# Performance work log

Hardware: AMD Instinct MI355X
Metric: run time of the kernel (lower is better)

Reference implementation:

```python
import jax, jax.numpy as jnp
import numpy as np

N = 50000          # num nodes
E = 800000         # num edges (avg degree 16)
F_IN = 512         # num_feature
HID = 128          # hid
COM_LAMBDA = 1.0


def setup_inputs() -> dict:
    key = jax.random.key(0)
    k1, k2, k3, k4, k5, k6 = jax.random.split(key, 6)
    v_ori_vals = jax.random.uniform(k1, (E,), dtype=jnp.float32)
    feat = jax.random.normal(k2, (N, F_IN), dtype=jnp.float32)
    v_indices = jax.random.randint(k3, (2, E), 0, N, dtype=jnp.int64)
    # GraphConvolution params
    gcn_w = jax.random.normal(k4, (F_IN, HID), dtype=jnp.float32) / np.sqrt(F_IN)
    gcn_b = jnp.zeros((HID,), dtype=jnp.float32)
    # gen_mlp: Linear(2*hid, 1), xavier_normal init
    std = 1.414 * np.sqrt(2.0 / (2 * HID + 1))
    mlp_w = jax.random.normal(k5, (1, 2 * HID), dtype=jnp.float32) * std
    mlp_b = jnp.zeros((1,), dtype=jnp.float32)
    return {"v_ori_vals": v_ori_vals, "feat": feat, "v_indices": v_indices,
            "num_node": N, "gcn_w": gcn_w, "gcn_b": gcn_b,
            "mlp_w": mlp_w, "mlp_b": mlp_b}


def reference(v_ori_vals, feat, v_indices, num_node, gcn_w, gcn_b, mlp_w, mlp_b):
    row, col = v_indices[0], v_indices[1]
    # gen_gcn: emb = A @ (feat @ W) + b  (SpMM via segment_sum over edges)
    support = feat @ gcn_w                                      # [N, HID]
    emb = jax.ops.segment_sum(v_ori_vals[:, None] * support[col], row,
                              num_segments=num_node) + gcn_b    # [N, HID]
    # gather endpoints, concat, edge-scoring MLP (dropout = identity in eval)
    ff = jnp.concatenate([emb[row], emb[col]], axis=-1)         # [E, 2*HID]
    temp = (ff @ mlp_w.T + mlp_b).reshape(-1)                   # [E]
    # sparse row-wise softmax over columns (dim=1) -> segment softmax by row
    m = jax.ops.segment_max(temp, row, num_segments=num_node)   # [N]
    e = jnp.exp(temp - m[row])                                  # [E]
    s = jax.ops.segment_sum(e, row, num_segments=num_node)      # [N]
    pi = e / s[row]                                             # [E]
    # gen_v = v_ori + com_lambda * pi (values on the shared edge pattern)
    return v_ori_vals + COM_LAMBDA * pi
```

## Files before the change

kernel.cpp:

```cpp
#include <hip/hip_runtime.h>


typedef unsigned int u32;

#define RPB     128
#define CAP     3072
#define NB_MAX  512
#define SB      256

__global__ void k_prep(const float* __restrict__ W, const float* __restrict__ mw,
                       float* __restrict__ u2, u32* __restrict__ cnt,
                       int F, int H, int nb) {
  if (blockIdx.x == 0)
    for (int s = threadIdx.x; s < nb; s += blockDim.x) cnt[s] = 0;
  int f = blockIdx.x * blockDim.x + threadIdx.x;
  if (f >= F) return;
  const float* wr = W + (size_t)f * H;
  float s = 0.f;
  for (int h = 0; h < H; ++h) s = fmaf(wr[h], mw[H + h], s);
  u2[f] = s;
}

template <int F>
__global__ void k_gemv(const float* __restrict__ feat, const float* __restrict__ u2,
                       float* __restrict__ q, int N) {
  const int lane = threadIdx.x & 63;
  const int sub  = lane & 15;
  const int grp  = lane >> 4;
  const int wid  = (blockIdx.x * blockDim.x + threadIdx.x) >> 6;
  const int r    = wid * 4 + grp;
  float4 uf[F / 64];
#pragma unroll
  for (int i = 0; i < F / 64; ++i)
    uf[i] = *(const float4*)(u2 + i * 64 + sub * 4);
  float a = 0.f;
  if (r < N) {
    const float* fr = feat + (size_t)r * F;
#pragma unroll
    for (int i = 0; i < F / 64; ++i) {
      float4 v = *(const float4*)(fr + i * 64 + sub * 4);
      a = fmaf(v.x, uf[i].x, fmaf(v.y, uf[i].y,
          fmaf(v.z, uf[i].z, fmaf(v.w, uf[i].w, a))));
    }
  }
  a += __shfl_xor(a, 8);
  a += __shfl_xor(a, 4);
  a += __shfl_xor(a, 2);
  a += __shfl_xor(a, 1);
  if (sub == 0 && r < N) q[r] = a;
}

__global__ void __launch_bounds__(1024)
k_sortscatter(const int* __restrict__ row, const int* __restrict__ col,
              const float* __restrict__ v, int E, int chunk,
              u32* __restrict__ cnt, uint2* __restrict__ rec8,
              u32* __restrict__ recE, int nb) {
  __shared__ u32 h[NB_MAX];
  __shared__ u32 start[NB_MAX];
  const int tid = threadIdx.x;
  for (int s = tid; s < nb; s += blockDim.x) h[s] = 0;
  __syncthreads();
  const int lo = blockIdx.x * chunk;
  const int hi = min(E, lo + chunk);
  for (int e = lo + tid; e < hi; e += blockDim.x)
    atomicAdd(&h[row[e] >> 7], 1u);
  __syncthreads();
  for (int s = tid; s < nb; s += blockDim.x) {
    u32 c = h[s];
    start[s] = c ? atomicAdd(&cnt[s], c) : 0u;
    h[s] = 0u;
  }
  __syncthreads();
  for (int e = lo + tid; e < hi; e += blockDim.x) {
    int r = row[e];
    int b = r >> 7;
    u32 rank = atomicAdd(&h[b], 1u);
    u32 slot = (u32)b * CAP + start[b] + rank;
    rec8[slot] = make_uint2(((u32)col[e] << 7) | (u32)(r & 127),
                            __float_as_uint(v[e]));
    recE[slot] = (u32)e;
  }
}

__global__ void __launch_bounds__(1024)
k_sum_t(const uint2* __restrict__ rec8, const u32* __restrict__ cnt,
        const float* __restrict__ q, float* __restrict__ t) {
  __shared__ float acc[RPB];
  const int b = blockIdx.x;
  const int tid = threadIdx.x;
  if (tid < RPB) acc[tid] = 0.f;
  __syncthreads();
  const u32 lo = (u32)b * CAP;
  const u32 hi = lo + min(cnt[b], (u32)CAP);
  for (u32 i = lo + tid; i < hi; i += blockDim.x) {
    uint2 rr = rec8[i];
    atomicAdd(&acc[rr.x & 127], q[rr.x >> 7] * __uint_as_float(rr.y));
  }
  __syncthreads();
  if (tid < RPB) t[b * RPB + tid] = __expf(acc[tid]);
}

__global__ void __launch_bounds__(1024)
k_sum_S_out(const uint2* __restrict__ rec8, const u32* __restrict__ recE,
            const u32* __restrict__ cnt, const float* __restrict__ t,
            const float* __restrict__ vori, float* __restrict__ out) {
  __shared__ float acc[RPB];
  const int b = blockIdx.x;
  const int tid = threadIdx.x;
  if (tid < RPB) acc[tid] = 0.f;
  __syncthreads();
  const u32 lo = (u32)b * CAP;
  const u32 hi = lo + min(cnt[b], (u32)CAP);
  for (u32 i = lo + tid; i < hi; i += blockDim.x) {
    uint2 rr = rec8[i];
    atomicAdd(&acc[rr.x & 127], t[rr.x >> 7]);
  }
  __syncthreads();
  if (tid < RPB) acc[tid] = 1.0f / acc[tid];
  __syncthreads();
  for (u32 i = lo + tid; i < hi; i += blockDim.x) {
    uint2 rr = rec8[i];
    u32 e = recE[i];
    out[e] = vori[e] + t[rr.x >> 7] * acc[rr.x & 127];
  }
}

__global__ void k_scatter_B_at(const int* __restrict__ row, const int* __restrict__ col,
                               const float* __restrict__ v, const float* __restrict__ q,
                               float* __restrict__ B, int E) {
  int e = blockIdx.x * blockDim.x + threadIdx.x;
  if (e >= E) return;
  atomicAdd(&B[row[e]], v[e] * q[col[e]]);
}
__global__ void k_node_t(const float* __restrict__ B, float* __restrict__ t, int N) {
  int n = blockIdx.x * blockDim.x + threadIdx.x;
  if (n < N) t[n] = __expf(B[n]);
}
__global__ void k_scatter_S_at(const int* __restrict__ row, const int* __restrict__ col,
                               const float* __restrict__ t, float* __restrict__ S, int E) {
  int e = blockIdx.x * blockDim.x + threadIdx.x;
  if (e >= E) return;
  atomicAdd(&S[row[e]], t[col[e]]);
}
__global__ void k_out_fb(const int* __restrict__ row, const int* __restrict__ col,
                         const float* __restrict__ vori, const float* __restrict__ t,
                         const float* __restrict__ S, float* __restrict__ out, int E) {
  int e = blockIdx.x * blockDim.x + threadIdx.x;
  if (e >= E) return;
  out[e] = vori[e] + t[col[e]] / S[row[e]];
}

extern "C" void kernel_launch(void* const* d_in, const int* in_sizes, int n_in,
                              void* d_out, int out_size, void* d_ws, size_t ws_size,
                              hipStream_t stream) {
  const float* vori = (const float*)d_in[0];
  const float* feat = (const float*)d_in[1];
  const int*   vind = (const int*)d_in[2];
  const float* W    = (const float*)d_in[4];
  const float* mw   = (const float*)d_in[6];

  const int E = in_sizes[0];
  const int H = in_sizes[6] / 2;
  const int F = in_sizes[4] / H;
  const int N = in_sizes[1] / F;

  const int* row = vind;
  const int* col = vind + E;

  const int nb   = (N + RPB - 1) / RPB;
  const int npad = nb * RPB;

  float* ws   = (float*)d_ws;
  float* u2   = ws;
  float* q    = u2 + F;
  float* t    = q + N;
  u32*   cnt  = (u32*)(t + npad);
  size_t hdr  = (size_t)((char*)(cnt + nb) - (char*)d_ws);
  hdr = (hdr + 15) & ~(size_t)15;
  uint2* rec8 = (uint2*)((char*)d_ws + hdr);
  u32*  recE  = (u32*)(rec8 + (size_t)nb * CAP);
  size_t need = hdr + (size_t)nb * CAP * 12u;

  k_prep<<<(F + 255) / 256, 256, 0, stream>>>(W, mw, u2, cnt, F, H, nb);
  k_gemv<512><<<(N + 15) / 16, 256, 0, stream>>>(feat, u2, q, N);

  if (ws_size >= need && F == 512 && nb <= NB_MAX) {
    const int chunk = (E + SB - 1) / SB;
    k_sortscatter<<<SB, 1024, 0, stream>>>(row, col, vori, E, chunk,
                                           cnt, rec8, recE, nb);
    k_sum_t<<<nb, 1024, 0, stream>>>(rec8, cnt, q, t);
    k_sum_S_out<<<nb, 1024, 0, stream>>>(rec8, recE, cnt, t, vori,
                                         (float*)d_out);
  } else {
    const int eb  = (E + 255) / 256;
    const int nbk = (N + 255) / 256;
    float* S = t + npad;
    hipMemsetAsync((void*)S, 0, sizeof(float) * (size_t)npad, stream);
    float* B = S;
    k_scatter_B_at<<<eb, 256, 0, stream>>>(row, col, vori, q, B, E);
    k_node_t<<<nbk, 256, 0, stream>>>(B, t, N);
    hipMemsetAsync((void*)S, 0, sizeof(float) * (size_t)npad, stream);
    k_scatter_S_at<<<eb, 256, 0, stream>>>(row, col, t, S, E);
    k_out_fb<<<eb, 256, 0, stream>>>(row, col, vori, t, S, (float*)d_out, E);
  }
}
```

Before: 246.9 us.

## Fuse all stages into one cooperative persistent kernel with grid syncs

Replaces the five-kernel pipeline (prep, gemv, sort-scatter, sum_t, sum_S_out) with a single cooperative kernel that runs 256 blocks of 1024 threads and separates the stages with grid.sync(). It drops the per-edge recE index buffer and writes the output with a direct per-edge pass that uses a stored inverse row sum. The aim is to remove launch gaps and the extra index traffic. In exchange it adds grid-wide barriers, runs the gemv and the per-bucket passes with a fixed, lower block count, and makes the final pass do random gathers on col and row.

```diff
diff --git a/kernel.cpp b/kernel.cpp
--- a/kernel.cpp
+++ b/kernel.cpp
@@ -1,4 +1,7 @@
 #include <hip/hip_runtime.h>
+#include <hip/hip_cooperative_groups.h>
+
+namespace cg = cooperative_groups;
 
 
 typedef unsigned int u32;
@@ -6,125 +9,153 @@
 #define RPB     128
 #define CAP     3072
 #define NB_MAX  512
-#define SB      256
-
-__global__ void k_prep(const float* __restrict__ W, const float* __restrict__ mw,
-                       float* __restrict__ u2, u32* __restrict__ cnt,
-                       int F, int H, int nb) {
-  if (blockIdx.x == 0)
-    for (int s = threadIdx.x; s < nb; s += blockDim.x) cnt[s] = 0;
+#define MBLK    256
+#define MTHR    1024
+
+template <int F>
+__global__ void __launch_bounds__(MTHR, 1)
+k_mega(const int* __restrict__ row, const int* __restrict__ col,
+       const float* __restrict__ vori, const float* __restrict__ feat,
+       const float* __restrict__ W, const float* __restrict__ mw,
+       float* __restrict__ u2, float* __restrict__ q,
+       float* __restrict__ t, float* __restrict__ invS,
+       u32* __restrict__ cnt, uint2* __restrict__ rec8,
+       float* __restrict__ out, int E, int N, int H, int nb) {
+  cg::grid_group grid = cg::this_grid();
+  const int tid  = threadIdx.x;
+  const int gtid = blockIdx.x * blockDim.x + tid;
+  const int gsz  = gridDim.x * blockDim.x;
+
+  __shared__ u32 h[NB_MAX];
+  __shared__ u32 start[NB_MAX];
+  __shared__ float acc[RPB];
+
+  for (int s = gtid; s < nb; s += gsz) cnt[s] = 0;
+  for (int f = gtid; f < F; f += gsz) {
+    const float* wr = W + (size_t)f * H;
+    float s = 0.f;
+    for (int hh = 0; hh < H; ++hh) s = fmaf(wr[hh], mw[H + hh], s);
+    u2[f] = s;
+  }
+  __threadfence();
+  grid.sync();
+
+  {
+    const int lane = tid & 63;
+    const int sub  = lane & 15;
+    const int grp  = lane >> 4;
+    const int wid  = gtid >> 6;
+    const int nwav = gsz >> 6;
+    float4 uf[F / 64];
+#pragma unroll
+    for (int i = 0; i < F / 64; ++i)
+      uf[i] = *(const float4*)(u2 + i * 64 + sub * 4);
+    for (int quad = wid; quad * 4 < N; quad += nwav) {
+      int r = quad * 4 + grp;
+      float a = 0.f;
+      if (r < N) {
+        const float* fr = feat + (size_t)r * F;
+#pragma unroll
+        for (int i = 0; i < F / 64; ++i) {
+          float4 v4 = *(const float4*)(fr + i * 64 + sub * 4);
+          a = fmaf(v4.x, uf[i].x, fmaf(v4.y, uf[i].y,
+              fmaf(v4.z, uf[i].z, fmaf(v4.w, uf[i].w, a))));
+        }
+      }
+      a += __shfl_xor(a, 8);
+      a += __shfl_xor(a, 4);
+      a += __shfl_xor(a, 2);
+      a += __shfl_xor(a, 1);
+      if (sub == 0 && r < N) q[r] = a;
+    }
+  }
+  __threadfence();
+  grid.sync();
+
+  {
+    const int chunk = (E + gridDim.x - 1) / gridDim.x;
+    for (int s = tid; s < nb; s += blockDim.x) h[s] = 0;
+    __syncthreads();
+    const int lo = blockIdx.x * chunk;
+    const int hi = min(E, lo + chunk);
+    for (int e = lo + tid; e < hi; e += blockDim.x)
+      atomicAdd(&h[row[e] >> 7], 1u);
+    __syncthreads();
+    for (int s = tid; s < nb; s += blockDim.x) {
+      u32 c = h[s];
+      start[s] = c ? atomicAdd(&cnt[s], c) : 0u;
+      h[s] = 0u;
+    }
+    __syncthreads();
+    for (int e = lo + tid; e < hi; e += blockDim.x) {
+      int r = row[e];
+      int b = r >> 7;
+      u32 rank = atomicAdd(&h[b], 1u);
+      u32 off  = min(start[b] + rank, (u32)CAP - 1);
+      rec8[(size_t)b * CAP + off] =
+          make_uint2(((u32)col[e] << 7) | (u32)(r & 127),
+                     __float_as_uint(vori[e]));
+    }
+  }
+  __threadfence();
+  grid.sync();
+
+  for (int b = blockIdx.x; b < nb; b += gridDim.x) {
+    if (tid < RPB) acc[tid] = 0.f;
+    __syncthreads();
+    const u32 lo = (u32)b * CAP;
+    const u32 n  = min(cnt[b], (u32)CAP);
+    for (u32 i = tid; i < n; i += blockDim.x) {
+      uint2 rr = rec8[lo + i];
+      atomicAdd(&acc[rr.x & 127], q[rr.x >> 7] * __uint_as_float(rr.y));
+    }
+    __syncthreads();
+    if (tid < RPB) t[b * RPB + tid] = __expf(acc[tid]);
+    __syncthreads();
+  }
+  __threadfence();
+  grid.sync();
+
+  for (int b = blockIdx.x; b < nb; b += gridDim.x) {
+    if (tid < RPB) acc[tid] = 0.f;
+    __syncthreads();
+    const u32 lo = (u32)b * CAP;
+    const u32 n  = min(cnt[b], (u32)CAP);
+    for (u32 i = tid; i < n; i += blockDim.x) {
+      uint2 rr = rec8[lo + i];
+      atomicAdd(&acc[rr.x & 127], t[rr.x >> 7]);
+    }
+    __syncthreads();
+    if (tid < RPB) invS[b * RPB + tid] = 1.0f / acc[tid];
+    __syncthreads();
+  }
+  __threadfence();
+  grid.sync();
+
+  for (int e = gtid; e < E; e += gsz)
+    out[e] = vori[e] + t[col[e]] * invS[row[e]];
+}
+
+__global__ void k_prep_fb(const float* __restrict__ W, const float* __restrict__ mw,
+                          float* __restrict__ u2, int F, int H) {
   int f = blockIdx.x * blockDim.x + threadIdx.x;
   if (f >= F) return;
   const float* wr = W + (size_t)f * H;
   float s = 0.f;
-  for (int h = 0; h < H; ++h) s = fmaf(wr[h], mw[H + h], s);
+  for (int hh = 0; hh < H; ++hh) s = fmaf(wr[hh], mw[H + hh], s);
   u2[f] = s;
 }
-
-template <int F>
-__global__ void k_gemv(const float* __restrict__ feat, const float* __restrict__ u2,
-                       float* __restrict__ q, int N) {
+__global__ void k_gemv_fb(const float* __restrict__ feat, const float* __restrict__ u2,
+                          float* __restrict__ q, int N, int F) {
   const int lane = threadIdx.x & 63;
-  const int sub  = lane & 15;
-  const int grp  = lane >> 4;
-  const int wid  = (blockIdx.x * blockDim.x + threadIdx.x) >> 6;
-  const int r    = wid * 4 + grp;
-  float4 uf[F / 64];
-#pragma unroll
-  for (int i = 0; i < F / 64; ++i)
-    uf[i] = *(const float4*)(u2 + i * 64 + sub * 4);
+  const int wave = (blockIdx.x * blockDim.x + threadIdx.x) >> 6;
+  if (wave >= N) return;
+  const float* fr = feat + (size_t)wave * F;
   float a = 0.f;
-  if (r < N) {
-    const float* fr = feat + (size_t)r * F;
-#pragma unroll
-    for (int i = 0; i < F / 64; ++i) {
-      float4 v = *(const float4*)(fr + i * 64 + sub * 4);
-      a = fmaf(v.x, uf[i].x, fmaf(v.y, uf[i].y,
-          fmaf(v.z, uf[i].z, fmaf(v.w, uf[i].w, a))));
-    }
-  }
-  a += __shfl_xor(a, 8);
-  a += __shfl_xor(a, 4);
-  a += __shfl_xor(a, 2);
-  a += __shfl_xor(a, 1);
-  if (sub == 0 && r < N) q[r] = a;
-}
-
-__global__ void __launch_bounds__(1024)
-k_sortscatter(const int* __restrict__ row, const int* __restrict__ col,
-              const float* __restrict__ v, int E, int chunk,
-              u32* __restrict__ cnt, uint2* __restrict__ rec8,
-              u32* __restrict__ recE, int nb) {
-  __shared__ u32 h[NB_MAX];
-  __shared__ u32 start[NB_MAX];
-  const int tid = threadIdx.x;
-  for (int s = tid; s < nb; s += blockDim.x) h[s] = 0;
-  __syncthreads();
-  const int lo = blockIdx.x * chunk;
-  const int hi = min(E, lo + chunk);
-  for (int e = lo + tid; e < hi; e += blockDim.x)
-    atomicAdd(&h[row[e] >> 7], 1u);
-  __syncthreads();
-  for (int s = tid; s < nb; s += blockDim.x) {
-    u32 c = h[s];
-    start[s] = c ? atomicAdd(&cnt[s], c) : 0u;
-    h[s] = 0u;
-  }
-  __syncthreads();
-  for (int e = lo + tid; e < hi; e += blockDim.x) {
-    int r = row[e];
-    int b = r >> 7;
-    u32 rank = atomicAdd(&h[b], 1u);
-    u32 slot = (u32)b * CAP + start[b] + rank;
-    rec8[slot] = make_uint2(((u32)col[e] << 7) | (u32)(r & 127),
-                            __float_as_uint(v[e]));
-    recE[slot] = (u32)e;
-  }
-}
-
-__global__ void __launch_bounds__(1024)
-k_sum_t(const uint2* __restrict__ rec8, const u32* __restrict__ cnt,
-        const float* __restrict__ q, float* __restrict__ t) {
-  __shared__ float acc[RPB];
-  const int b = blockIdx.x;
-  const int tid = threadIdx.x;
-  if (tid < RPB) acc[tid] = 0.f;
-  __syncthreads();
-  const u32 lo = (u32)b * CAP;
-  const u32 hi = lo + min(cnt[b], (u32)CAP);
-  for (u32 i = lo + tid; i < hi; i += blockDim.x) {
-    uint2 rr = rec8[i];
-    atomicAdd(&acc[rr.x & 127], q[rr.x >> 7] * __uint_as_float(rr.y));
-  }
-  __syncthreads();
-  if (tid < RPB) t[b * RPB + tid] = __expf(acc[tid]);
-}
-
-__global__ void __launch_bounds__(1024)
-k_sum_S_out(const uint2* __restrict__ rec8, const u32* __restrict__ recE,
-            const u32* __restrict__ cnt, const float* __restrict__ t,
-            const float* __restrict__ vori, float* __restrict__ out) {
-  __shared__ float acc[RPB];
-  const int b = blockIdx.x;
-  const int tid = threadIdx.x;
-  if (tid < RPB) acc[tid] = 0.f;
-  __syncthreads();
-  const u32 lo = (u32)b * CAP;
-  const u32 hi = lo + min(cnt[b], (u32)CAP);
-  for (u32 i = lo + tid; i < hi; i += blockDim.x) {
-    uint2 rr = rec8[i];
-    atomicAdd(&acc[rr.x & 127], t[rr.x >> 7]);
-  }
-  __syncthreads();
-  if (tid < RPB) acc[tid] = 1.0f / acc[tid];
-  __syncthreads();
-  for (u32 i = lo + tid; i < hi; i += blockDim.x) {
-    uint2 rr = rec8[i];
-    u32 e = recE[i];
-    out[e] = vori[e] + t[rr.x >> 7] * acc[rr.x & 127];
-  }
-}
-
+  for (int i = lane; i < F; i += 64) a = fmaf(fr[i], u2[i], a);
+  for (int off = 32; off; off >>= 1) a += __shfl_xor(a, off);
+  if (lane == 0) q[wave] = a;
+}
 __global__ void k_scatter_B_at(const int* __restrict__ row, const int* __restrict__ col,
                                const float* __restrict__ v, const float* __restrict__ q,
                                float* __restrict__ B, int E) {
@@ -153,54 +184,56 @@
 extern "C" void kernel_launch(void* const* d_in, const int* in_sizes, int n_in,
                               void* d_out, int out_size, void* d_ws, size_t ws_size,
                               hipStream_t stream) {
-  const float* vori = (const float*)d_in[0];
-  const float* feat = (const float*)d_in[1];
-  const int*   vind = (const int*)d_in[2];
-  const float* W    = (const float*)d_in[4];
-  const float* mw   = (const float*)d_in[6];
+  const int*   row_p  = (const int*)d_in[2];
+  const float* vori_p = (const float*)d_in[0];
+  const float* feat_p = (const float*)d_in[1];
+  const float* W_p    = (const float*)d_in[4];
+  const float* mw_p   = (const float*)d_in[6];
 
   const int E = in_sizes[0];
   const int H = in_sizes[6] / 2;
   const int F = in_sizes[4] / H;
   const int N = in_sizes[1] / F;
 
-  const int* row = vind;
-  const int* col = vind + E;
+  const int* col_p = row_p + E;
 
   const int nb   = (N + RPB - 1) / RPB;
   const int npad = nb * RPB;
 
   float* ws   = (float*)d_ws;
-  float* u2   = ws;
-  float* q    = u2 + F;
-  float* t    = q + N;
-  u32*   cnt  = (u32*)(t + npad);
-  size_t hdr  = (size_t)((char*)(cnt + nb) - (char*)d_ws);
+  float* u2_p = ws;
+  float* q_p  = u2_p + F;
+  float* t_p  = q_p + N;
+  float* iS_p = t_p + npad;
+  u32*  cnt_p = (u32*)(iS_p + npad);
+  size_t hdr  = (size_t)((char*)(cnt_p + nb) - (char*)d_ws);
   hdr = (hdr + 15) & ~(size_t)15;
-  uint2* rec8 = (uint2*)((char*)d_ws + hdr);
-  u32*  recE  = (u32*)(rec8 + (size_t)nb * CAP);
-  size_t need = hdr + (size_t)nb * CAP * 12u;
-
-  k_prep<<<(F + 255) / 256, 256, 0, stream>>>(W, mw, u2, cnt, F, H, nb);
-  k_gemv<512><<<(N + 15) / 16, 256, 0, stream>>>(feat, u2, q, N);
+  uint2* rec_p = (uint2*)((char*)d_ws + hdr);
+  size_t need  = hdr + (size_t)nb * CAP * sizeof(uint2);
 
   if (ws_size >= need && F == 512 && nb <= NB_MAX) {
-    const int chunk = (E + SB - 1) / SB;
-    k_sortscatter<<<SB, 1024, 0, stream>>>(row, col, vori, E, chunk,
-                                           cnt, rec8, recE, nb);
-    k_sum_t<<<nb, 1024, 0, stream>>>(rec8, cnt, q, t);
-    k_sum_S_out<<<nb, 1024, 0, stream>>>(rec8, recE, cnt, t, vori,
-                                         (float*)d_out);
+    float* out_p = (float*)d_out;
+    int E_ = E, N_ = N, H_ = H, nb_ = nb;
+    void* args[] = {
+      (void*)&row_p, (void*)&col_p, (void*)&vori_p, (void*)&feat_p,
+      (void*)&W_p,   (void*)&mw_p,  (void*)&u2_p,   (void*)&q_p,
+      (void*)&t_p,   (void*)&iS_p,  (void*)&cnt_p,  (void*)&rec_p,
+      (void*)&out_p, (void*)&E_,    (void*)&N_,     (void*)&H_,
+      (void*)&nb_
+    };
+    hipLaunchCooperativeKernel((const void*)k_mega<512>, dim3(MBLK), dim3(MTHR),
+                               args, 0, stream);
   } else {
     const int eb  = (E + 255) / 256;
     const int nbk = (N + 255) / 256;
-    float* S = t + npad;
+    float* S = iS_p;
+    k_prep_fb<<<(F + 255) / 256, 256, 0, stream>>>(W_p, mw_p, u2_p, F, H);
+    k_gemv_fb<<<(N * 64 + 255) / 256, 256, 0, stream>>>(feat_p, u2_p, q_p, N, F);
     hipMemsetAsync((void*)S, 0, sizeof(float) * (size_t)npad, stream);
-    float* B = S;
-    k_scatter_B_at<<<eb, 256, 0, stream>>>(row, col, vori, q, B, E);
-    k_node_t<<<nbk, 256, 0, stream>>>(B, t, N);
+    k_scatter_B_at<<<eb, 256, 0, stream>>>(row_p, col_p, vori_p, q_p, S, E);
+    k_node_t<<<nbk, 256, 0, stream>>>(S, t_p, N);
     hipMemsetAsync((void*)S, 0, sizeof(float) * (size_t)npad, stream);
-    k_scatter_S_at<<<eb, 256, 0, stream>>>(row, col, t, S, E);
-    k_out_fb<<<eb, 256, 0, stream>>>(row, col, vori, t, S, (float*)d_out, E);
-  }
-}
+    k_scatter_S_at<<<eb, 256, 0, stream>>>(row_p, col_p, t_p, S, E);
+    k_out_fb<<<eb, 256, 0, stream>>>(row_p, col_p, vori_p, t_p, S, (float*)d_out, E);
+  }
+}
```

Measured after the change: 831.9 us. 3.37x slower.

## Drop edge-id records, write output in edge order, use grid-stride GEMV

Applied to the files above, without the earlier changes.

Removes the per-edge recE index array from the bucketed records. The final pass now computes 1/S per node in a reduction kernel and writes the output in a separate coalesced edge-order kernel that gathers t[col] and invS[row], replacing the scattered out[e] writes. The GEMV now gives one whole wavefront per feature row with a fixed grid-stride launch, and k_prep reads with vectorized float4 loads. Record offsets are clamped to CAP-1 to avoid overflow, at the cost of an extra kernel launch and re-reading row/col indices.

```diff
diff --git a/kernel.cpp b/kernel.cpp
--- a/kernel.cpp
+++ b/kernel.cpp
@@ -15,9 +15,13 @@
     for (int s = threadIdx.x; s < nb; s += blockDim.x) cnt[s] = 0;
   int f = blockIdx.x * blockDim.x + threadIdx.x;
   if (f >= F) return;
-  const float* wr = W + (size_t)f * H;
+  const float4* wr = (const float4*)(W + (size_t)f * H);
+  const float4* mv = (const float4*)(mw + H);
   float s = 0.f;
-  for (int h = 0; h < H; ++h) s = fmaf(wr[h], mw[H + h], s);
+  for (int i = 0; i < H / 4; ++i) {
+    float4 a = wr[i], b = mv[i];
+    s = fmaf(a.x, b.x, fmaf(a.y, b.y, fmaf(a.z, b.z, fmaf(a.w, b.w, s))));
+  }
   u2[f] = s;
 }
 
@@ -25,36 +29,31 @@
 __global__ void k_gemv(const float* __restrict__ feat, const float* __restrict__ u2,
                        float* __restrict__ q, int N) {
   const int lane = threadIdx.x & 63;
-  const int sub  = lane & 15;
-  const int grp  = lane >> 4;
-  const int wid  = (blockIdx.x * blockDim.x + threadIdx.x) >> 6;
-  const int r    = wid * 4 + grp;
-  float4 uf[F / 64];
-#pragma unroll
-  for (int i = 0; i < F / 64; ++i)
-    uf[i] = *(const float4*)(u2 + i * 64 + sub * 4);
-  float a = 0.f;
-  if (r < N) {
-    const float* fr = feat + (size_t)r * F;
-#pragma unroll
-    for (int i = 0; i < F / 64; ++i) {
-      float4 v = *(const float4*)(fr + i * 64 + sub * 4);
-      a = fmaf(v.x, uf[i].x, fmaf(v.y, uf[i].y,
-          fmaf(v.z, uf[i].z, fmaf(v.w, uf[i].w, a))));
-    }
-  }
-  a += __shfl_xor(a, 8);
-  a += __shfl_xor(a, 4);
-  a += __shfl_xor(a, 2);
-  a += __shfl_xor(a, 1);
-  if (sub == 0 && r < N) q[r] = a;
+  const float4 ua = *(const float4*)(u2 + lane * 8);
+  const float4 ub = *(const float4*)(u2 + lane * 8 + 4);
+  const int wid = (blockIdx.x * blockDim.x + threadIdx.x) >> 6;
+  const int nw  = (gridDim.x * blockDim.x) >> 6;
+  for (int r = wid; r < N; r += nw) {
+    const float* fr = feat + (size_t)r * F + lane * 8;
+    float4 a = *(const float4*)fr;
+    float4 b = *(const float4*)(fr + 4);
+    float s = fmaf(a.x, ua.x, fmaf(a.y, ua.y, fmaf(a.z, ua.z,
+              fmaf(a.w, ua.w, fmaf(b.x, ub.x, fmaf(b.y, ub.y,
+              fmaf(b.z, ub.z, b.w * ub.w)))))));
+    s += __shfl_xor(s, 32);
+    s += __shfl_xor(s, 16);
+    s += __shfl_xor(s, 8);
+    s += __shfl_xor(s, 4);
+    s += __shfl_xor(s, 2);
+    s += __shfl_xor(s, 1);
+    if (lane == 0) q[r] = s;
+  }
 }
 
 __global__ void __launch_bounds__(1024)
 k_sortscatter(const int* __restrict__ row, const int* __restrict__ col,
               const float* __restrict__ v, int E, int chunk,
-              u32* __restrict__ cnt, uint2* __restrict__ rec8,
-              u32* __restrict__ recE, int nb) {
+              u32* __restrict__ cnt, uint2* __restrict__ rec8, int nb) {
   __shared__ u32 h[NB_MAX];
   __shared__ u32 start[NB_MAX];
   const int tid = threadIdx.x;
@@ -75,10 +74,10 @@
     int r = row[e];
     int b = r >> 7;
     u32 rank = atomicAdd(&h[b], 1u);
-    u32 slot = (u32)b * CAP + start[b] + rank;
-    rec8[slot] = make_uint2(((u32)col[e] << 7) | (u32)(r & 127),
-                            __float_as_uint(v[e]));
-    recE[slot] = (u32)e;
+    u32 off  = min(start[b] + rank, (u32)CAP - 1);
+    rec8[(size_t)b * CAP + off] =
+        make_uint2(((u32)col[e] << 7) | (u32)(r & 127),
+                   __float_as_uint(v[e]));
   }
 }
 
@@ -91,9 +90,9 @@
   if (tid < RPB) acc[tid] = 0.f;
   __syncthreads();
   const u32 lo = (u32)b * CAP;
-  const u32 hi = lo + min(cnt[b], (u32)CAP);
-  for (u32 i = lo + tid; i < hi; i += blockDim.x) {
-    uint2 rr = rec8[i];
+  const u32 n  = min(cnt[b], (u32)CAP);
+  for (u32 i = tid; i < n; i += blockDim.x) {
+    uint2 rr = rec8[lo + i];
     atomicAdd(&acc[rr.x & 127], q[rr.x >> 7] * __uint_as_float(rr.y));
   }
   __syncthreads();
@@ -101,28 +100,30 @@
 }
 
 __global__ void __launch_bounds__(1024)
-k_sum_S_out(const uint2* __restrict__ rec8, const u32* __restrict__ recE,
-            const u32* __restrict__ cnt, const float* __restrict__ t,
-            const float* __restrict__ vori, float* __restrict__ out) {
+k_sum_invS(const uint2* __restrict__ rec8, const u32* __restrict__ cnt,
+           const float* __restrict__ t, float* __restrict__ invS) {
   __shared__ float acc[RPB];
   const int b = blockIdx.x;
   const int tid = threadIdx.x;
   if (tid < RPB) acc[tid] = 0.f;
   __syncthreads();
   const u32 lo = (u32)b * CAP;
-  const u32 hi = lo + min(cnt[b], (u32)CAP);
-  for (u32 i = lo + tid; i < hi; i += blockDim.x) {
-    uint2 rr = rec8[i];
+  const u32 n  = min(cnt[b], (u32)CAP);
+  for (u32 i = tid; i < n; i += blockDim.x) {
+    uint2 rr = rec8[lo + i];
     atomicAdd(&acc[rr.x & 127], t[rr.x >> 7]);
   }
   __syncthreads();
-  if (tid < RPB) acc[tid] = 1.0f / acc[tid];
-  __syncthreads();
-  for (u32 i = lo + tid; i < hi; i += blockDim.x) {
-    uint2 rr = rec8[i];
-    u32 e = recE[i];
-    out[e] = vori[e] + t[rr.x >> 7] * acc[rr.x & 127];
-  }
+  if (tid < RPB) invS[b * RPB + tid] = 1.0f / acc[tid];
+}
+
+__global__ void k_out(const int* __restrict__ row, const int* __restrict__ col,
+                      const float* __restrict__ vori, const float* __restrict__ t,
+                      const float* __restrict__ invS, float* __restrict__ out,
+                      int E) {
+  int e = blockIdx.x * blockDim.x + threadIdx.x;
+  if (e >= E) return;
+  out[e] = vori[e] + t[col[e]] * invS[row[e]];
 }
 
 __global__ void k_scatter_B_at(const int* __restrict__ row, const int* __restrict__ col,
@@ -142,9 +143,9 @@
   if (e >= E) return;
   atomicAdd(&S[row[e]], t[col[e]]);
 }
-__global__ void k_out_fb(const int* __restrict__ row, const int* __restrict__ col,
-                         const float* __restrict__ vori, const float* __restrict__ t,
-                         const float* __restrict__ S, float* __restrict__ out, int E) {
+__global__ void k_out_div(const int* __restrict__ row, const int* __restrict__ col,
+                          const float* __restrict__ vori, const float* __restrict__ t,
+                          const float* __restrict__ S, float* __restrict__ out, int E) {
   int e = blockIdx.x * blockDim.x + threadIdx.x;
   if (e >= E) return;
   out[e] = vori[e] + t[col[e]] / S[row[e]];
@@ -174,33 +175,32 @@
   float* u2   = ws;
   float* q    = u2 + F;
   float* t    = q + N;
-  u32*   cnt  = (u32*)(t + npad);
+  float* invS = t + npad;
+  u32*   cnt  = (u32*)(invS + npad);
   size_t hdr  = (size_t)((char*)(cnt + nb) - (char*)d_ws);
   hdr = (hdr + 15) & ~(size_t)15;
   uint2* rec8 = (uint2*)((char*)d_ws + hdr);
-  u32*  recE  = (u32*)(rec8 + (size_t)nb * CAP);
-  size_t need = hdr + (size_t)nb * CAP * 12u;
+  size_t need = hdr + (size_t)nb * CAP * sizeof(uint2);
+
+  const int eb = (E + 255) / 256;
 
   k_prep<<<(F + 255) / 256, 256, 0, stream>>>(W, mw, u2, cnt, F, H, nb);
-  k_gemv<512><<<(N + 15) / 16, 256, 0, stream>>>(feat, u2, q, N);
-
-  if (ws_size >= need && F == 512 && nb <= NB_MAX) {
+  k_gemv<512><<<3125, 256, 0, stream>>>(feat, u2, q, N);
+
+  if (ws_size >= need && F == 512 && H % 4 == 0 && nb <= NB_MAX) {
     const int chunk = (E + SB - 1) / SB;
-    k_sortscatter<<<SB, 1024, 0, stream>>>(row, col, vori, E, chunk,
-                                           cnt, rec8, recE, nb);
+    k_sortscatter<<<SB, 1024, 0, stream>>>(row, col, vori, E, chunk, cnt, rec8, nb);
     k_sum_t<<<nb, 1024, 0, stream>>>(rec8, cnt, q, t);
-    k_sum_S_out<<<nb, 1024, 0, stream>>>(rec8, recE, cnt, t, vori,
-                                         (float*)d_out);
+    k_sum_invS<<<nb, 1024, 0, stream>>>(rec8, cnt, t, invS);
+    k_out<<<eb, 256, 0, stream>>>(row, col, vori, t, invS, (float*)d_out, E);
   } else {
-    const int eb  = (E + 255) / 256;
     const int nbk = (N + 255) / 256;
-    float* S = t + npad;
+    float* S = invS;
     hipMemsetAsync((void*)S, 0, sizeof(float) * (size_t)npad, stream);
-    float* B = S;
-    k_scatter_B_at<<<eb, 256, 0, stream>>>(row, col, vori, q, B, E);
-    k_node_t<<<nbk, 256, 0, stream>>>(B, t, N);
+    k_scatter_B_at<<<eb, 256, 0, stream>>>(row, col, vori, q, S, E);
+    k_node_t<<<nbk, 256, 0, stream>>>(S, t, N);
     hipMemsetAsync((void*)S, 0, sizeof(float) * (size_t)npad, stream);
     k_scatter_S_at<<<eb, 256, 0, stream>>>(row, col, t, S, E);
-    k_out_fb<<<eb, 256, 0, stream>>>(row, col, vori, t, S, (float*)d_out, E);
-  }
-}
+    k_out_div<<<eb, 256, 0, stream>>>(row, col, vori, t, S, (float*)d_out, E);
+  }
+}
```

After: 217.1 us. 1.14x faster.
